# Performance work log

Hardware: AMD Instinct MI355X
Metric: run time of the kernel (lower is better)

The kernel has to match this reference:

```python
import jax, jax.numpy as jnp
import numpy as np

MOMENTUM = 0.9
COMMITMENT_COST = 0.25
EPS = 1e-20


def setup_inputs() -> dict:
    key = jax.random.key(0)
    k1, k2 = jax.random.split(key)
    D, K = 512, 8192
    B, S = 16, 512
    x = jax.random.normal(k1, (B, S, D), dtype=jnp.float32)
    # variance_scaling(1.0, 'fan_in', 'uniform') on shape (D, K): fan_in = D
    limit = np.sqrt(3.0 / D).astype(np.float32)
    e = jax.random.uniform(k2, (D, K), dtype=jnp.float32, minval=-limit, maxval=limit)
    cs = jnp.zeros((K,), dtype=jnp.float32)
    un = jnp.zeros((D, K), dtype=jnp.float32)
    return {"x": x, "e": e, "cs": cs, "un": un}


def reference(x, e, cs, un):
    D, K = e.shape
    input_shape = x.shape[:-1]            # (B, S)
    xf = x.reshape(-1, D)                 # (N, D)
    # pairwise squared distances: (N, K)
    dist = (jnp.sum(xf * xf, axis=1, keepdims=True)
            + jnp.sum(e * e, axis=0, keepdims=True)
            - 2.0 * xf @ e)
    enc_idx = jnp.argmax(-dist, axis=1)                      # (N,)
    enc = jax.nn.one_hot(enc_idx, K, dtype=x.dtype)          # (N, K)
    quantized = jnp.take(e.T, enc_idx, axis=0).reshape(*input_shape, D)

    # EMA codebook update (train=True branch)
    new_cs = (1.0 - MOMENTUM) * jnp.sum(enc, axis=0) + MOMENTUM * cs
    new_un = (1.0 - MOMENTUM) * (xf.T @ enc) + MOMENTUM * un
    n = jnp.sum(new_cs)
    stable_cs = (new_cs + EPS) / (n + K * EPS) * n
    new_e = new_un / stable_cs[None, :]

    loss = COMMITMENT_COST * jnp.mean((jax.lax.stop_gradient(quantized) - x) ** 2)
    quantized_st = x + jax.lax.stop_gradient(quantized - x)  # straight-through

    avg_probs = jnp.mean(enc.reshape(*input_shape, K), axis=0)           # (S, K)
    over_latents = jnp.mean(avg_probs, axis=tuple(range(len(input_shape) - 1)))  # (K,)
    perplexity = jnp.exp(-jnp.sum(over_latents * jnp.log(over_latents + EPS)))
    return quantized_st, loss, perplexity, enc_idx, new_e, new_cs, new_un
```

## Files before the change

### kernel.cpp

```cpp
#include <hip/hip_runtime.h>
#include <math.h>

#define D_ 512
#define K_ 8192
#define N_ 8192
#define KSLICES 16
#define NCAND (KSLICES * 4)
#define TAU 0.01f

typedef _Float16 f16x8 __attribute__((ext_vector_type(8)));
typedef __attribute__((ext_vector_type(4))) float f32x4;

__global__ void xprep_kernel(const float* __restrict__ x, _Float16* __restrict__ xf,
                             float* __restrict__ x2f) {
    __shared__ float xs[2048];
    const int tid = threadIdx.x;
    const size_t base = (size_t)blockIdx.x * 2048;
    float4 a = *(const float4*)&x[base + tid * 8];
    float4 b = *(const float4*)&x[base + tid * 8 + 4];
    f16x8 h;
    h[0] = (_Float16)a.x; h[1] = (_Float16)a.y; h[2] = (_Float16)a.z; h[3] = (_Float16)a.w;
    h[4] = (_Float16)b.x; h[5] = (_Float16)b.y; h[6] = (_Float16)b.z; h[7] = (_Float16)b.w;
    *(f16x8*)&xf[base + tid * 8] = h;
    *(float4*)&xs[tid * 8] = a;
    *(float4*)&xs[tid * 8 + 4] = b;
    __syncthreads();
    if (tid < 128) {
        const int l = tid & 63;
        const int row = ((tid >> 6) << 1) + (l >> 5);
        const int c = l & 31;
        const int blk = c >> 3, j = c & 7;
        const float* rb = &xs[row * 512 + blk * 128];
        float v0 = rb[j];
        float r = __fmul_rn(v0, v0);
        for (int i = 8; i < 128; i += 8) {
            float v = rb[i + j];
            r = __fadd_rn(r, __fmul_rn(v, v));
        }
        r = __fadd_rn(r, __shfl_xor(r, 1));
        r = __fadd_rn(r, __shfl_xor(r, 2));
        r = __fadd_rn(r, __shfl_xor(r, 4));
        r = __fadd_rn(r, __shfl_xor(r, 8));
        r = __fadd_rn(r, __shfl_xor(r, 16));
        if (c == 0) x2f[blockIdx.x * 4 + row] = r;
    }
}

__global__ void e2f_kernel(const float* __restrict__ e, float* __restrict__ e2f) {
    int k = blockIdx.x * 64 + threadIdx.x;
    float s = 0.0f;
    #pragma unroll 4
    for (int d = 0; d < D_; ++d) {
        float v = e[(size_t)d * K_ + k];
        s = __fadd_rn(s, __fmul_rn(v, v));
    }
    e2f[k] = s;
}

__global__ void eprep_kernel(const float* __restrict__ e,
                             _Float16* __restrict__ efT, float* __restrict__ eT) {
    __shared__ float t[64][65];
    const int tid = threadIdx.x;
    const int k0 = blockIdx.x * 64;
    const int d0 = blockIdx.y * 64;
    #pragma unroll
    for (int it = 0; it < 4; ++it) {
        int dt = (tid >> 4) + it * 16;
        int c4 = (tid & 15) * 4;
        float4 v = *(const float4*)&e[(size_t)(d0 + dt) * K_ + k0 + c4];
        t[dt][c4 + 0] = v.x; t[dt][c4 + 1] = v.y; t[dt][c4 + 2] = v.z; t[dt][c4 + 3] = v.w;
    }
    __syncthreads();
    const int m = tid >> 2, ch = tid & 3;
    size_t o = (size_t)(k0 + m) * D_ + d0 + ch * 16;
    f16x8 h0, h1;
    #pragma unroll
    for (int j = 0; j < 8; ++j) h0[j] = (_Float16)t[ch * 16 + j][m];
    #pragma unroll
    for (int j = 0; j < 8; ++j) h1[j] = (_Float16)t[ch * 16 + 8 + j][m];
    *(f16x8*)&efT[o] = h0;
    *(f16x8*)&efT[o + 8] = h1;
    #pragma unroll
    for (int j4 = 0; j4 < 4; ++j4) {
        float4 w;
        w.x = t[ch * 16 + j4 * 4 + 0][m];
        w.y = t[ch * 16 + j4 * 4 + 1][m];
        w.z = t[ch * 16 + j4 * 4 + 2][m];
        w.w = t[ch * 16 + j4 * 4 + 3][m];
        *(float4*)&eT[o + j4 * 4] = w;
    }
}

__launch_bounds__(256, 2)
__global__ void argmin_mfma(const _Float16* __restrict__ xf, const _Float16* __restrict__ efT,
                            const float* __restrict__ x2f, const float* __restrict__ e2f,
                            float* __restrict__ pv4, int* __restrict__ pi4) {
    __shared__ _Float16 XS[2][4096];
    __shared__ _Float16 ES[2][8192];
    __shared__ float e2s[256];

    const int tid = threadIdx.x;
    const int lane = tid & 63;
    const int wid = tid >> 6;
    const int wm = wid & 1, wn = wid >> 1;
    const int lidx = lane & 15, g = lane >> 4;
    const int rowbase = blockIdx.y * 128;
    const int kslice = blockIdx.x;

    float x2r[4];
    #pragma unroll
    for (int nt = 0; nt < 4; ++nt)
        x2r[nt] = x2f[rowbase + (wn << 6) + (nt << 4) + lidx];

    float best[4], sec[4]; int bi[4], si[4];
    #pragma unroll
    for (int nt = 0; nt < 4; ++nt) {
        best[nt] = 3.0e38f; sec[nt] = 3.0e38f; bi[nt] = 0x7ffffffe; si[nt] = 0x7fffffff;
    }

    const int fx0 = tid,       rx0 = fx0 >> 2, cx0 = ((fx0 & 3) - (rx0 >> 1)) & 3;
    const int fx1 = tid + 256, rx1 = fx1 >> 2, cx1 = ((fx1 & 3) - (rx1 >> 1)) & 3;
    const size_t xo0 = (size_t)(rowbase + rx0) * D_ + cx0 * 8;
    const size_t xo1 = (size_t)(rowbase + rx1) * D_ + cx1 * 8;
    int fe[4], re[4], ce[4];
    #pragma unroll
    for (int j = 0; j < 4; ++j) {
        fe[j] = tid + j * 256; re[j] = fe[j] >> 2; ce[j] = ((fe[j] & 3) - (re[j] >> 1)) & 3;
    }

    for (int cc = 0; cc < 2; ++cc) {
        const int codebase = kslice * 512 + cc * 256;
        __syncthreads();
        e2s[tid] = e2f[codebase + tid];

        f32x4 acc[8][4];
        const f32x4 z4 = {0.0f, 0.0f, 0.0f, 0.0f};
        #pragma unroll
        for (int mt = 0; mt < 8; ++mt)
            #pragma unroll
            for (int nt = 0; nt < 4; ++nt) acc[mt][nt] = z4;

        f16x8 st[6];
        st[0] = *(const f16x8*)&xf[xo0];
        st[1] = *(const f16x8*)&xf[xo1];
        #pragma unroll
        for (int j = 0; j < 4; ++j)
            st[2 + j] = *(const f16x8*)&efT[(size_t)(codebase + re[j]) * D_ + ce[j] * 8];
        *(f16x8*)&XS[0][fx0 * 8] = st[0];
        *(f16x8*)&XS[0][fx1 * 8] = st[1];
        #pragma unroll
        for (int j = 0; j < 4; ++j) *(f16x8*)&ES[0][fe[j] * 8] = st[2 + j];
        __syncthreads();

        #define STEP_PHASE(CUR, NXT, STEP)                                               \
        {                                                                                \
            if ((STEP) < 15) {                                                           \
                const int dd = ((STEP) + 1) << 5;                                        \
                st[0] = *(const f16x8*)&xf[xo0 + dd];                                    \
                st[1] = *(const f16x8*)&xf[xo1 + dd];                                    \
                _Pragma("unroll")                                                        \
                for (int j = 0; j < 4; ++j)                                              \
                    st[2 + j] = *(const f16x8*)&efT[(size_t)(codebase + re[j]) * D_ + dd + ce[j] * 8]; \
            }                                                                            \
            f16x8 bh[4];                                                                 \
            _Pragma("unroll")                                                            \
            for (int nt = 0; nt < 4; ++nt) {                                             \
                int n = (wn << 6) + (nt << 4) + lidx;                                    \
                int sb = (g + (n >> 1)) & 3;                                             \
                bh[nt] = *(const f16x8*)&XS[CUR][n * 32 + sb * 8];                       \
            }                                                                            \
            _Pragma("unroll")                                                            \
            for (int mt = 0; mt < 8; ++mt) {                                             \
                int m = (wm << 7) + (mt << 4) + lidx;                                    \
                int sa = (g + (m >> 1)) & 3;                                             \
                f16x8 ah = *(const f16x8*)&ES[CUR][m * 32 + sa * 8];                     \
                _Pragma("unroll")                                                        \
                for (int nt = 0; nt < 4; ++nt)                                           \
                    acc[mt][nt] = __builtin_amdgcn_mfma_f32_16x16x32_f16(ah, bh[nt], acc[mt][nt], 0, 0, 0); \
            }                                                                            \
            if ((STEP) < 15) {                                                           \
                *(f16x8*)&XS[NXT][fx0 * 8] = st[0];                                      \
                *(f16x8*)&XS[NXT][fx1 * 8] = st[1];                                      \
                _Pragma("unroll")                                                        \
                for (int j = 0; j < 4; ++j) *(f16x8*)&ES[NXT][fe[j] * 8] = st[2 + j];    \
            }                                                                            \
            __syncthreads();                                                             \
        }

        for (int s2 = 0; s2 < 8; ++s2) {
            STEP_PHASE(0, 1, s2 * 2)
            STEP_PHASE(1, 0, s2 * 2 + 1)
        }
        #undef STEP_PHASE

        #pragma unroll
        for (int mt = 0; mt < 8; ++mt) {
            #pragma unroll
            for (int r = 0; r < 4; ++r) {
                const int ml = (wm << 7) + (mt << 4) + (g << 2) + r;
                const float e2k = e2s[ml];
                const int kg = codebase + ml;
                #pragma unroll
                for (int nt = 0; nt < 4; ++nt) {
                    float dot = acc[mt][nt][r];
                    float s = __fsub_rn(__fadd_rn(x2r[nt], e2k), __fmul_rn(2.0f, dot));
                    if (s < best[nt]) {
                        sec[nt] = best[nt]; si[nt] = bi[nt];
                        best[nt] = s; bi[nt] = kg;
                    } else if (s < sec[nt]) {
                        sec[nt] = s; si[nt] = kg;
                    }
                }
            }
        }
    }

    __syncthreads();
    float* entV = (float*)XS;
    int*   entI = (int*)ES;
    #pragma unroll
    for (int nt = 0; nt < 4; ++nt) {
        int rl = (wn << 6) + (nt << 4) + lidx;
        int slot = ((wm << 2) + g) << 1;
        entV[rl * 16 + slot] = best[nt];  entI[rl * 16 + slot] = bi[nt];
        entV[rl * 16 + slot + 1] = sec[nt]; entI[rl * 16 + slot + 1] = si[nt];
    }
    __syncthreads();
    if (tid < 128) {
        float v4[4] = {3.0e38f, 3.0e38f, 3.0e38f, 3.0e38f};
        int i4[4] = {0x7fffffff, 0x7fffffff, 0x7fffffff, 0x7fffffff};
        #pragma unroll
        for (int t2 = 0; t2 < 16; ++t2) {
            float v = entV[tid * 16 + t2]; int i = entI[tid * 16 + t2];
            #pragma unroll
            for (int p = 0; p < 4; ++p) {
                bool better = (v < v4[p]) || (v == v4[p] && i < i4[p]);
                if (better) {
                    float tv = v4[p]; v4[p] = v; v = tv;
                    int ti = i4[p]; i4[p] = i; i = ti;
                }
            }
        }
        size_t o = (size_t)(rowbase + tid) * NCAND + kslice * 4;
        #pragma unroll
        for (int p = 0; p < 4; ++p) { pv4[o + p] = v4[p]; pi4[o + p] = i4[p]; }
    }
}

__global__ void argmin_reduce(const float* __restrict__ pv4, const int* __restrict__ pi4,
                              int* __restrict__ idxbuf, float* __restrict__ out_idx,
                              int* __restrict__ flaglist, unsigned* __restrict__ nflag,
                              unsigned* __restrict__ counts) {
    int n = blockIdx.x * 256 + threadIdx.x;
    float bv = 3.0e38f, sv = 3.0e38f; int bi = 0x7fffffff;
    for (int j = 0; j < NCAND; ++j) {
        float v = pv4[(size_t)n * NCAND + j]; int i = pi4[(size_t)n * NCAND + j];
        if (v < bv || (v == bv && i < bi)) { sv = bv; bv = v; bi = i; }
        else if (v < sv) sv = v;
    }
    idxbuf[n] = bi;
    out_idx[n] = (float)bi;
    if (sv - bv < TAU) {
        unsigned pos = atomicAdd(nflag, 1u);
        flaglist[pos] = n;
    } else {
        atomicAdd(&counts[bi], 1u);
    }
}

__launch_bounds__(256, 2)
__global__ void refine_kernel(const float* __restrict__ x, const float* __restrict__ eT,
                              const float* __restrict__ x2f, const float* __restrict__ e2f,
                              const int* __restrict__ flaglist, const unsigned* __restrict__ nflag,
                              const int* __restrict__ pi4,
                              int* __restrict__ idxbuf, float* __restrict__ out_idx,
                              unsigned* __restrict__ counts) {
    __shared__ float xrow[D_];
    __shared__ double part[NCAND][4];
    __shared__ int candi[NCAND];
    __shared__ float sv[NCAND];
    const int tid = threadIdx.x;
    const unsigned nf = *nflag;
    for (unsigned f = blockIdx.x; f < nf; f += gridDim.x) {
        const int n = flaglist[f];
        __syncthreads();
        if (tid < NCAND) candi[tid] = pi4[(size_t)n * NCAND + tid];
        for (int d = tid; d < D_; d += 256) xrow[d] = x[(size_t)n * D_ + d];
        __syncthreads();
        const int c = tid >> 2, j = tid & 3;
        const int k = candi[c];
        double a = 0.0;
        #pragma unroll 8
        for (int d = j; d < D_; d += 4)
            a = fma((double)xrow[d], (double)eT[(size_t)k * D_ + d], a);
        part[c][j] = a;
        __syncthreads();
        if (j == 0) {
            double dot = (part[c][0] + part[c][1]) + (part[c][2] + part[c][3]);
            float md = (float)dot;
            sv[c] = __fsub_rn(__fadd_rn(x2f[n], e2f[k]), __fmul_rn(2.0f, md));
        }
        __syncthreads();
        if (tid == 0) {
            float bv = 3.0e38f; int bi = 0x7fffffff;
            for (int c2 = 0; c2 < NCAND; ++c2) {
                float v = sv[c2]; int i2 = candi[c2];
                if (v < bv || (v == bv && i2 < bi)) { bv = v; bi = i2; }
            }
            idxbuf[n] = bi; out_idx[n] = (float)bi;
            atomicAdd(&counts[bi], 1u);
        }
        __syncthreads();
    }
}

__global__ void scan_kernel(const unsigned* __restrict__ counts,
                            unsigned* __restrict__ offsets, unsigned* __restrict__ cursor) {
    __shared__ unsigned ps[256];
    const int t = threadIdx.x;
    const int base = t * 32;
    unsigned s = 0;
    for (int j = 0; j < 32; ++j) s += counts[base + j];
    ps[t] = s;
    __syncthreads();
    for (int off = 1; off < 256; off <<= 1) {
        unsigned v = (t >= off) ? ps[t - off] : 0u;
        __syncthreads();
        ps[t] += v;
        __syncthreads();
    }
    unsigned run = (t > 0) ? ps[t - 1] : 0u;
    for (int j = 0; j < 32; ++j) {
        int k = base + j;
        offsets[k] = run;
        cursor[k] = run;
        run += counts[k];
    }
}

__global__ void fill_kernel(const int* __restrict__ idxbuf, unsigned* __restrict__ cursor,
                            int* __restrict__ rowlist) {
    int n = blockIdx.x * 256 + threadIdx.x;
    int k = idxbuf[n];
    unsigned pos = atomicAdd(&cursor[k], 1u);
    rowlist[pos] = n;
}

__global__ void quant_loss_kernel(const float* __restrict__ x, const float* __restrict__ eT,
                                  const int* __restrict__ idxbuf,
                                  float* __restrict__ qout, double* __restrict__ loss_part) {
    int n = blockIdx.x;
    int k = idxbuf[n];
    int d = threadIdx.x * 2;
    float2 q = *(const float2*)&eT[(size_t)k * D_ + d];
    float2 xv = *(const float2*)&x[(size_t)n * D_ + d];
    float2 o;
    float dfx = q.x - xv.x, dfy = q.y - xv.y;
    o.x = xv.x + dfx; o.y = xv.y + dfy;
    *(float2*)&qout[(size_t)n * D_ + d] = o;
    double part = fma((double)dfx, (double)dfx, (double)dfy * (double)dfy);
    __shared__ double sr[256];
    sr[threadIdx.x] = part;
    __syncthreads();
    for (int s = 128; s > 0; s >>= 1) {
        if (threadIdx.x < s) sr[threadIdx.x] += sr[threadIdx.x + s];
        __syncthreads();
    }
    if (threadIdx.x == 0) loss_part[n] = sr[0];
}

__global__ void cs_kernel(const unsigned* __restrict__ counts, const float* __restrict__ cs,
                          float* __restrict__ out_cs,
                          double* __restrict__ ncs_part, double* __restrict__ ent_part) {
    int tid = threadIdx.x;
    int k = blockIdx.x * 256 + tid;
    float cnt = (float)counts[k];
    float ncs = 0.1f * cnt + 0.9f * cs[k];
    out_cs[k] = ncs;
    double p = (double)counts[k] / 8192.0;
    double ent = -p * log(p + 1e-20);

    __shared__ double s1[256], s2[256];
    s1[tid] = (double)ncs;
    s2[tid] = ent;
    __syncthreads();
    for (int s = 128; s > 0; s >>= 1) {
        if (tid < s) { s1[tid] += s1[tid + s]; s2[tid] += s2[tid + s]; }
        __syncthreads();
    }
    if (tid == 0) { ncs_part[blockIdx.x] = s1[0]; ent_part[blockIdx.x] = s2[0]; }
}

__global__ void scalars_kernel(const double* __restrict__ loss_part,
                               const double* __restrict__ ncs_part,
                               const double* __restrict__ ent_part,
                               float* __restrict__ out_loss, float* __restrict__ out_ppl,
                               double* __restrict__ nsum_out) {
    __shared__ double sr[256];
    double s = 0.0;
    for (int i = threadIdx.x; i < N_; i += 256) s += loss_part[i];
    sr[threadIdx.x] = s;
    __syncthreads();
    for (int t = 128; t > 0; t >>= 1) {
        if (threadIdx.x < t) sr[threadIdx.x] += sr[threadIdx.x + t];
        __syncthreads();
    }
    if (threadIdx.x == 0) {
        out_loss[0] = (float)(0.25 * (sr[0] / (double)((size_t)N_ * D_)));
        double nsum = 0.0, ent = 0.0;
        for (int i = 0; i < 32; ++i) { nsum += ncs_part[i]; ent += ent_part[i]; }
        out_ppl[0] = (float)exp(ent);
        nsum_out[0] = nsum;
    }
}

__global__ void merge_kernel(const float* __restrict__ x, const float* __restrict__ un,
                             const float* __restrict__ out_cs,
                             const unsigned* __restrict__ offsets, const unsigned* __restrict__ counts,
                             const int* __restrict__ rowlist, const double* __restrict__ nsum,
                             float* __restrict__ out_un, float* __restrict__ out_e) {
    const int f = blockIdx.x * 256 + threadIdx.x;
    const int k = f & (K_ - 1);
    const int d0 = (f >> 13) * 4;
    const unsigned start = offsets[k];
    const unsigned cnt = counts[k];
    float4 s = {0.0f, 0.0f, 0.0f, 0.0f};
    for (unsigned i = 0; i < cnt; ++i) {
        int nr = rowlist[start + i];
        const float4 v = *(const float4*)&x[(size_t)nr * D_ + d0];
        s.x += v.x; s.y += v.y; s.z += v.z; s.w += v.w;
    }
    const double nn = nsum[0];
    const double denom = nn + 8192.0 * 1e-20;
    const float scs = (float)((((double)out_cs[k] + 1e-20) / denom) * nn);
    const float sv[4] = {s.x, s.y, s.z, s.w};
    #pragma unroll
    for (int j = 0; j < 4; ++j) {
        size_t o = (size_t)(d0 + j) * K_ + k;
        float uval = 0.9f * un[o] + 0.1f * sv[j];
        out_un[o] = uval;
        out_e[o] = uval / scs;
    }
}

extern "C" void kernel_launch(void* const* d_in, const int* in_sizes, int n_in,
                              void* d_out, int out_size, void* d_ws, size_t ws_size,
                              hipStream_t stream) {
    const float* x  = (const float*)d_in[0];
    const float* e  = (const float*)d_in[1];
    const float* cs = (const float*)d_in[2];
    const float* un = (const float*)d_in[3];

    float* out = (float*)d_out;
    float* out_q    = out;
    float* out_loss = out + 4194304;
    float* out_ppl  = out + 4194305;
    float* out_idx  = out + 4194306;
    float* out_e    = out + 4202498;
    float* out_cs   = out + 8396802;
    float* out_un   = out + 8404994;

    _Float16* xf16 = (_Float16*)out_q;
    float* pv4 = (float*)(out_q + 2097152);
    int*   pi4 = (int*)(out_q + 2621440);
    _Float16* efT  = (_Float16*)out_e;
    float* eT = (float*)out_un;

    char* ws = (char*)d_ws;
    unsigned* counts  = (unsigned*)ws;
    unsigned* nflag   = (unsigned*)(ws + 32768);
    float* x2f        = (float*)(ws + 36864);
    float* e2f        = (float*)(ws + 69632);
    int*   idxbuf     = (int*)(ws + 102400);
    int*   flaglist   = (int*)(ws + 135168);
    double* loss_part = (double*)(ws + 167936);
    double* ncs_part  = (double*)(ws + 233472);
    double* ent_part  = (double*)(ws + 233728);
    double* nsum      = (double*)(ws + 233984);
    unsigned* offsets = (unsigned*)(ws + 234240);
    unsigned* cursor  = (unsigned*)(ws + 267008);
    int*   rowlist    = (int*)(ws + 299776);

    hipMemsetAsync(d_ws, 0, 36864, stream);
    xprep_kernel<<<2048, 256, 0, stream>>>(x, xf16, x2f);
    eprep_kernel<<<dim3(K_ / 64, D_ / 64), 256, 0, stream>>>(e, efT, eT);
    e2f_kernel<<<K_ / 64, 64, 0, stream>>>(e, e2f);
    argmin_mfma<<<dim3(KSLICES, N_ / 128), 256, 0, stream>>>(xf16, efT, x2f, e2f, pv4, pi4);
    argmin_reduce<<<N_ / 256, 256, 0, stream>>>(pv4, pi4, idxbuf, out_idx, flaglist, nflag, counts);
    refine_kernel<<<256, 256, 0, stream>>>(x, eT, x2f, e2f, flaglist, nflag, pi4, idxbuf, out_idx, counts);
    scan_kernel<<<1, 256, 0, stream>>>(counts, offsets, cursor);
    fill_kernel<<<N_ / 256, 256, 0, stream>>>(idxbuf, cursor, rowlist);
    quant_loss_kernel<<<N_, 256, 0, stream>>>(x, eT, idxbuf, out_q, loss_part);
    cs_kernel<<<K_ / 256, 256, 0, stream>>>(counts, cs, out_cs, ncs_part, ent_part);
    scalars_kernel<<<1, 256, 0, stream>>>(loss_part, ncs_part, ent_part, out_loss, out_ppl, nsum);
    merge_kernel<<<K_ * (D_ / 4) / 256, 256, 0, stream>>>(x, un, out_cs, offsets, counts, rowlist, nsum, out_un, out_e);
}
```

Before: 243.9 us.

## Split argmin over 32 code slices and fuse cs stats into scan kernel

The argmin GEMM now uses 32 K-slices of 256 codes per block instead of 16 slices of 512, doubling grid size so more blocks can run in parallel and dropping the inner two-chunk loop. Candidates per row double to 128, so the refine kernel now uses two threads per candidate and the candidate buffer is moved to fit. The codebook-size/entropy computation is folded into the single-block scan kernel, removing the separate cs kernel and its partial buffers. In exchange the argmin reduction and refine stages process twice as many candidates, and the fused scan runs serially in one block.

```diff
diff --git a/kernel.cpp b/kernel.cpp
--- a/kernel.cpp
+++ b/kernel.cpp
@@ -4,7 +4,7 @@
 #define D_ 512
 #define K_ 8192
 #define N_ 8192
-#define KSLICES 16
+#define KSLICES 32
 #define NCAND (KSLICES * 4)
 #define TAU 0.01f
 
@@ -106,6 +106,7 @@
     const int lidx = lane & 15, g = lane >> 4;
     const int rowbase = blockIdx.y * 128;
     const int kslice = blockIdx.x;
+    const int codebase = kslice * 256;
 
     float x2r[4];
     #pragma unroll
@@ -128,88 +129,84 @@
         fe[j] = tid + j * 256; re[j] = fe[j] >> 2; ce[j] = ((fe[j] & 3) - (re[j] >> 1)) & 3;
     }
 
-    for (int cc = 0; cc < 2; ++cc) {
-        const int codebase = kslice * 512 + cc * 256;
-        __syncthreads();
-        e2s[tid] = e2f[codebase + tid];
-
-        f32x4 acc[8][4];
-        const f32x4 z4 = {0.0f, 0.0f, 0.0f, 0.0f};
+    e2s[tid] = e2f[codebase + tid];
+
+    f32x4 acc[8][4];
+    const f32x4 z4 = {0.0f, 0.0f, 0.0f, 0.0f};
+    #pragma unroll
+    for (int mt = 0; mt < 8; ++mt)
         #pragma unroll
-        for (int mt = 0; mt < 8; ++mt)
+        for (int nt = 0; nt < 4; ++nt) acc[mt][nt] = z4;
+
+    f16x8 st[6];
+    st[0] = *(const f16x8*)&xf[xo0];
+    st[1] = *(const f16x8*)&xf[xo1];
+    #pragma unroll
+    for (int j = 0; j < 4; ++j)
+        st[2 + j] = *(const f16x8*)&efT[(size_t)(codebase + re[j]) * D_ + ce[j] * 8];
+    *(f16x8*)&XS[0][fx0 * 8] = st[0];
+    *(f16x8*)&XS[0][fx1 * 8] = st[1];
+    #pragma unroll
+    for (int j = 0; j < 4; ++j) *(f16x8*)&ES[0][fe[j] * 8] = st[2 + j];
+    __syncthreads();
+
+    #define STEP_PHASE(CUR, NXT, STEP)                                               \
+    {                                                                                \
+        if ((STEP) < 15) {                                                           \
+            const int dd = ((STEP) + 1) << 5;                                        \
+            st[0] = *(const f16x8*)&xf[xo0 + dd];                                    \
+            st[1] = *(const f16x8*)&xf[xo1 + dd];                                    \
+            _Pragma("unroll")                                                        \
+            for (int j = 0; j < 4; ++j)                                              \
+                st[2 + j] = *(const f16x8*)&efT[(size_t)(codebase + re[j]) * D_ + dd + ce[j] * 8]; \
+        }                                                                            \
+        f16x8 bh[4];                                                                 \
+        _Pragma("unroll")                                                            \
+        for (int nt = 0; nt < 4; ++nt) {                                             \
+            int n = (wn << 6) + (nt << 4) + lidx;                                    \
+            int sb = (g + (n >> 1)) & 3;                                             \
+            bh[nt] = *(const f16x8*)&XS[CUR][n * 32 + sb * 8];                       \
+        }                                                                            \
+        _Pragma("unroll")                                                            \
+        for (int mt = 0; mt < 8; ++mt) {                                             \
+            int m = (wm << 7) + (mt << 4) + lidx;                                    \
+            int sa = (g + (m >> 1)) & 3;                                             \
+            f16x8 ah = *(const f16x8*)&ES[CUR][m * 32 + sa * 8];                     \
+            _Pragma("unroll")                                                        \
+            for (int nt = 0; nt < 4; ++nt)                                           \
+                acc[mt][nt] = __builtin_amdgcn_mfma_f32_16x16x32_f16(ah, bh[nt], acc[mt][nt], 0, 0, 0); \
+        }                                                                            \
+        if ((STEP) < 15) {                                                           \
+            *(f16x8*)&XS[NXT][fx0 * 8] = st[0];                                      \
+            *(f16x8*)&XS[NXT][fx1 * 8] = st[1];                                      \
+            _Pragma("unroll")                                                        \
+            for (int j = 0; j < 4; ++j) *(f16x8*)&ES[NXT][fe[j] * 8] = st[2 + j];    \
+        }                                                                            \
+        __syncthreads();                                                             \
+    }
+
+    for (int s2 = 0; s2 < 8; ++s2) {
+        STEP_PHASE(0, 1, s2 * 2)
+        STEP_PHASE(1, 0, s2 * 2 + 1)
+    }
+    #undef STEP_PHASE
+
+    #pragma unroll
+    for (int mt = 0; mt < 8; ++mt) {
+        #pragma unroll
+        for (int r = 0; r < 4; ++r) {
+            const int ml = (wm << 7) + (mt << 4) + (g << 2) + r;
+            const float e2k = e2s[ml];
+            const int kg = codebase + ml;
             #pragma unroll
-            for (int nt = 0; nt < 4; ++nt) acc[mt][nt] = z4;
-
-        f16x8 st[6];
-        st[0] = *(const f16x8*)&xf[xo0];
-        st[1] = *(const f16x8*)&xf[xo1];
-        #pragma unroll
-        for (int j = 0; j < 4; ++j)
-            st[2 + j] = *(const f16x8*)&efT[(size_t)(codebase + re[j]) * D_ + ce[j] * 8];
-        *(f16x8*)&XS[0][fx0 * 8] = st[0];
-        *(f16x8*)&XS[0][fx1 * 8] = st[1];
-        #pragma unroll
-        for (int j = 0; j < 4; ++j) *(f16x8*)&ES[0][fe[j] * 8] = st[2 + j];
-        __syncthreads();
-
-        #define STEP_PHASE(CUR, NXT, STEP)                                               \
-        {                                                                                \
-            if ((STEP) < 15) {                                                           \
-                const int dd = ((STEP) + 1) << 5;                                        \
-                st[0] = *(const f16x8*)&xf[xo0 + dd];                                    \
-                st[1] = *(const f16x8*)&xf[xo1 + dd];                                    \
-                _Pragma("unroll")                                                        \
-                for (int j = 0; j < 4; ++j)                                              \
-                    st[2 + j] = *(const f16x8*)&efT[(size_t)(codebase + re[j]) * D_ + dd + ce[j] * 8]; \
-            }                                                                            \
-            f16x8 bh[4];                                                                 \
-            _Pragma("unroll")                                                            \
-            for (int nt = 0; nt < 4; ++nt) {                                             \
-                int n = (wn << 6) + (nt << 4) + lidx;                                    \
-                int sb = (g + (n >> 1)) & 3;                                             \
-                bh[nt] = *(const f16x8*)&XS[CUR][n * 32 + sb * 8];                       \
-            }                                                                            \
-            _Pragma("unroll")                                                            \
-            for (int mt = 0; mt < 8; ++mt) {                                             \
-                int m = (wm << 7) + (mt << 4) + lidx;                                    \
-                int sa = (g + (m >> 1)) & 3;                                             \
-                f16x8 ah = *(const f16x8*)&ES[CUR][m * 32 + sa * 8];                     \
-                _Pragma("unroll")                                                        \
-                for (int nt = 0; nt < 4; ++nt)                                           \
-                    acc[mt][nt] = __builtin_amdgcn_mfma_f32_16x16x32_f16(ah, bh[nt], acc[mt][nt], 0, 0, 0); \
-            }                                                                            \
-            if ((STEP) < 15) {                                                           \
-                *(f16x8*)&XS[NXT][fx0 * 8] = st[0];                                      \
-                *(f16x8*)&XS[NXT][fx1 * 8] = st[1];                                      \
-                _Pragma("unroll")                                                        \
-                for (int j = 0; j < 4; ++j) *(f16x8*)&ES[NXT][fe[j] * 8] = st[2 + j];    \
-            }                                                                            \
-            __syncthreads();                                                             \
-        }
-
-        for (int s2 = 0; s2 < 8; ++s2) {
-            STEP_PHASE(0, 1, s2 * 2)
-            STEP_PHASE(1, 0, s2 * 2 + 1)
-        }
-        #undef STEP_PHASE
-
-        #pragma unroll
-        for (int mt = 0; mt < 8; ++mt) {
-            #pragma unroll
-            for (int r = 0; r < 4; ++r) {
-                const int ml = (wm << 7) + (mt << 4) + (g << 2) + r;
-                const float e2k = e2s[ml];
-                const int kg = codebase + ml;
-                #pragma unroll
-                for (int nt = 0; nt < 4; ++nt) {
-                    float dot = acc[mt][nt][r];
-                    float s = __fsub_rn(__fadd_rn(x2r[nt], e2k), __fmul_rn(2.0f, dot));
-                    if (s < best[nt]) {
-                        sec[nt] = best[nt]; si[nt] = bi[nt];
-                        best[nt] = s; bi[nt] = kg;
-                    } else if (s < sec[nt]) {
-                        sec[nt] = s; si[nt] = kg;
-                    }
+            for (int nt = 0; nt < 4; ++nt) {
+                float dot = acc[mt][nt][r];
+                float s = __fsub_rn(__fadd_rn(x2r[nt], e2k), __fmul_rn(2.0f, dot));
+                if (s < best[nt]) {
+                    sec[nt] = best[nt]; si[nt] = bi[nt];
+                    best[nt] = s; bi[nt] = kg;
+                } else if (s < sec[nt]) {
+                    sec[nt] = s; si[nt] = kg;
                 }
             }
         }
@@ -276,7 +273,7 @@
                               int* __restrict__ idxbuf, float* __restrict__ out_idx,
                               unsigned* __restrict__ counts) {
     __shared__ float xrow[D_];
-    __shared__ double part[NCAND][4];
+    __shared__ double part[NCAND][2];
     __shared__ int candi[NCAND];
     __shared__ float sv[NCAND];
     const int tid = threadIdx.x;
@@ -287,16 +284,16 @@
         if (tid < NCAND) candi[tid] = pi4[(size_t)n * NCAND + tid];
         for (int d = tid; d < D_; d += 256) xrow[d] = x[(size_t)n * D_ + d];
         __syncthreads();
-        const int c = tid >> 2, j = tid & 3;
+        const int c = tid >> 1, j = tid & 1;
         const int k = candi[c];
         double a = 0.0;
         #pragma unroll 8
-        for (int d = j; d < D_; d += 4)
+        for (int d = j; d < D_; d += 2)
             a = fma((double)xrow[d], (double)eT[(size_t)k * D_ + d], a);
         part[c][j] = a;
         __syncthreads();
         if (j == 0) {
-            double dot = (part[c][0] + part[c][1]) + (part[c][2] + part[c][3]);
+            double dot = part[c][0] + part[c][1];
             float md = (float)dot;
             sv[c] = __fsub_rn(__fadd_rn(x2f[n], e2f[k]), __fmul_rn(2.0f, md));
         }
@@ -314,14 +311,27 @@
     }
 }
 
-__global__ void scan_kernel(const unsigned* __restrict__ counts,
-                            unsigned* __restrict__ offsets, unsigned* __restrict__ cursor) {
+__global__ void cs_scan_kernel(const unsigned* __restrict__ counts, const float* __restrict__ cs,
+                               float* __restrict__ out_cs,
+                               unsigned* __restrict__ offsets, unsigned* __restrict__ cursor,
+                               float* __restrict__ out_ppl, double* __restrict__ nsum_out) {
     __shared__ unsigned ps[256];
+    __shared__ double s1[256], s2[256];
     const int t = threadIdx.x;
     const int base = t * 32;
-    unsigned s = 0;
-    for (int j = 0; j < 32; ++j) s += counts[base + j];
-    ps[t] = s;
+    unsigned scnt = 0;
+    double ncs_sum = 0.0, ent_sum = 0.0;
+    for (int j = 0; j < 32; ++j) {
+        int k = base + j;
+        unsigned cnt = counts[k];
+        scnt += cnt;
+        float ncs = 0.1f * (float)cnt + 0.9f * cs[k];
+        out_cs[k] = ncs;
+        ncs_sum += (double)ncs;
+        double p = (double)cnt / 8192.0;
+        ent_sum += -p * log(p + 1e-20);
+    }
+    ps[t] = scnt; s1[t] = ncs_sum; s2[t] = ent_sum;
     __syncthreads();
     for (int off = 1; off < 256; off <<= 1) {
         unsigned v = (t >= off) ? ps[t - off] : 0u;
@@ -335,6 +345,14 @@
         offsets[k] = run;
         cursor[k] = run;
         run += counts[k];
+    }
+    for (int s = 128; s > 0; s >>= 1) {
+        if (t < s) { s1[t] += s1[t + s]; s2[t] += s2[t + s]; }
+        __syncthreads();
+    }
+    if (t == 0) {
+        nsum_out[0] = s1[0];
+        out_ppl[0] = (float)exp(s2[0]);
     }
 }
 
@@ -369,33 +387,8 @@
     if (threadIdx.x == 0) loss_part[n] = sr[0];
 }
 
-__global__ void cs_kernel(const unsigned* __restrict__ counts, const float* __restrict__ cs,
-                          float* __restrict__ out_cs,
-                          double* __restrict__ ncs_part, double* __restrict__ ent_part) {
-    int tid = threadIdx.x;
-    int k = blockIdx.x * 256 + tid;
-    float cnt = (float)counts[k];
-    float ncs = 0.1f * cnt + 0.9f * cs[k];
-    out_cs[k] = ncs;
-    double p = (double)counts[k] / 8192.0;
-    double ent = -p * log(p + 1e-20);
-
-    __shared__ double s1[256], s2[256];
-    s1[tid] = (double)ncs;
-    s2[tid] = ent;
-    __syncthreads();
-    for (int s = 128; s > 0; s >>= 1) {
-        if (tid < s) { s1[tid] += s1[tid + s]; s2[tid] += s2[tid + s]; }
-        __syncthreads();
-    }
-    if (tid == 0) { ncs_part[blockIdx.x] = s1[0]; ent_part[blockIdx.x] = s2[0]; }
-}
-
 __global__ void scalars_kernel(const double* __restrict__ loss_part,
-                               const double* __restrict__ ncs_part,
-                               const double* __restrict__ ent_part,
-                               float* __restrict__ out_loss, float* __restrict__ out_ppl,
-                               double* __restrict__ nsum_out) {
+                               float* __restrict__ out_loss) {
     __shared__ double sr[256];
     double s = 0.0;
     for (int i = threadIdx.x; i < N_; i += 256) s += loss_part[i];
@@ -405,13 +398,8 @@
         if (threadIdx.x < t) sr[threadIdx.x] += sr[threadIdx.x + t];
         __syncthreads();
     }
-    if (threadIdx.x == 0) {
+    if (threadIdx.x == 0)
         out_loss[0] = (float)(0.25 * (sr[0] / (double)((size_t)N_ * D_)));
-        double nsum = 0.0, ent = 0.0;
-        for (int i = 0; i < 32; ++i) { nsum += ncs_part[i]; ent += ent_part[i]; }
-        out_ppl[0] = (float)exp(ent);
-        nsum_out[0] = nsum;
-    }
 }
 
 __global__ void merge_kernel(const float* __restrict__ x, const float* __restrict__ un,
@@ -462,7 +450,7 @@
 
     _Float16* xf16 = (_Float16*)out_q;
     float* pv4 = (float*)(out_q + 2097152);
-    int*   pi4 = (int*)(out_q + 2621440);
+    int*   pi4 = (int*)(out_q + 3145728);
     _Float16* efT  = (_Float16*)out_e;
     float* eT = (float*)out_un;
 
@@ -474,8 +462,6 @@
     int*   idxbuf     = (int*)(ws + 102400);
     int*   flaglist   = (int*)(ws + 135168);
     double* loss_part = (double*)(ws + 167936);
-    double* ncs_part  = (double*)(ws + 233472);
-    double* ent_part  = (double*)(ws + 233728);
     double* nsum      = (double*)(ws + 233984);
     unsigned* offsets = (unsigned*)(ws + 234240);
     unsigned* cursor  = (unsigned*)(ws + 267008);
@@ -488,10 +474,9 @@
     argmin_mfma<<<dim3(KSLICES, N_ / 128), 256, 0, stream>>>(xf16, efT, x2f, e2f, pv4, pi4);
     argmin_reduce<<<N_ / 256, 256, 0, stream>>>(pv4, pi4, idxbuf, out_idx, flaglist, nflag, counts);
     refine_kernel<<<256, 256, 0, stream>>>(x, eT, x2f, e2f, flaglist, nflag, pi4, idxbuf, out_idx, counts);
-    scan_kernel<<<1, 256, 0, stream>>>(counts, offsets, cursor);
+    cs_scan_kernel<<<1, 256, 0, stream>>>(counts, cs, out_cs, offsets, cursor, out_ppl, nsum);
     fill_kernel<<<N_ / 256, 256, 0, stream>>>(idxbuf, cursor, rowlist);
     quant_loss_kernel<<<N_, 256, 0, stream>>>(x, eT, idxbuf, out_q, loss_part);
-    cs_kernel<<<K_ / 256, 256, 0, stream>>>(counts, cs, out_cs, ncs_part, ent_part);
-    scalars_kernel<<<1, 256, 0, stream>>>(loss_part, ncs_part, ent_part, out_loss, out_ppl, nsum);
+    scalars_kernel<<<1, 256, 0, stream>>>(loss_part, out_loss);
     merge_kernel<<<K_ * (D_ / 4) / 256, 256, 0, stream>>>(x, un, out_cs, offsets, counts, rowlist, nsum, out_un, out_e);
 }
```

Measured after the change: 309.2 us. +26.7%, slower.
